# Performance work log

Measured on AMD Instinct MI355X. Metric: run time of the kernel, lower is better.

## Reference

```python
import jax, jax.numpy as jnp
import numpy as np
from jax import lax

D_MODEL = 512
N_HEADS = 8
D_HEAD = D_MODEL // N_HEADS
MAX_LANDMARKS = 100


def setup_inputs() -> dict:
    key = jax.random.key(0)
    ks = jax.random.split(key, 12)
    B, L, D = 16, 8192, D_MODEL
    s = 1.0 / np.sqrt(D)
    return {
        "mamba_output": jax.random.normal(ks[0], (B, L, D), jnp.float32),
        "hawkes_skip": jax.random.normal(ks[1], (B, L, D), jnp.float32),
        "hawkes_weights": jax.random.uniform(ks[2], (B, L), jnp.float32),
        "Wq": jax.random.uniform(ks[3], (D, D), jnp.float32, -s, s),
        "bq": jax.random.uniform(ks[4], (D,), jnp.float32, -s, s),
        "Wk": jax.random.uniform(ks[5], (D, D), jnp.float32, -s, s),
        "bk": jax.random.uniform(ks[6], (D,), jnp.float32, -s, s),
        "Wv": jax.random.uniform(ks[7], (D, D), jnp.float32, -s, s),
        "bv": jax.random.uniform(ks[8], (D,), jnp.float32, -s, s),
        "Wo": jax.random.uniform(ks[9], (D, D), jnp.float32, -s, s),
        "bo": jax.random.uniform(ks[10], (D,), jnp.float32, -s, s),
    }


def reference(mamba_output, hawkes_skip, hawkes_weights,
              Wq, bq, Wk, bk, Wv, bv, Wo, bo):
    B, L, D = hawkes_skip.shape
    H, dh = N_HEADS, D_HEAD
    k = min(MAX_LANDMARKS, L)
    scale = dh ** (-0.5)

    # top-k landmark selection over sequence, then chronological sort
    _, idx = lax.top_k(hawkes_weights, k)          # (B, k)
    idx = jnp.sort(idx, axis=1)
    landmark_kv = jnp.take_along_axis(hawkes_skip, idx[:, :, None], axis=1)  # (B, k, D)

    # single query = last timestep of mamba output
    query = mamba_output[:, -1, :]                 # (B, D)
    Q = (query @ Wq.T + bq).reshape(B, H, dh)      # (B, H, dh)
    K = (landmark_kv @ Wk.T + bk).reshape(B, k, H, dh)
    V = (landmark_kv @ Wv.T + bv).reshape(B, k, H, dh)

    scores = jnp.einsum("bhd,bkhd->bhk", Q, K) * scale   # (B, H, k)
    probs = jax.nn.softmax(scores, axis=-1)
    attn = jnp.einsum("bhk,bkhd->bhd", probs, V).reshape(B, D)
    return attn @ Wo.T + bo                        # (B, D)
```

## Files before the change

kernel.cpp:

```cpp
#include <hip/hip_runtime.h>
#include <hip/hip_bf16.h>
#include <stdint.h>

#define B_SZ 16
#define L_SEQ 8192
#define D_MOD 512
#define N_H 8
#define D_H 64
#define KSEL 100

__global__ __launch_bounds__(512) void fused_attn_kernel(
    const float* __restrict__ mamba, const float* __restrict__ skip,
    const float* __restrict__ w,
    const float* __restrict__ Wq, const float* __restrict__ bq,
    const float* __restrict__ Wk, const float* __restrict__ bk,
    const float* __restrict__ Wv, const float* __restrict__ bv,
    const float* __restrict__ Wo, const float* __restrict__ bo,
    float* __restrict__ out) {
    const int b = blockIdx.x >> 3;
    const int h = blockIdx.x & 7;
    const int t = threadIdx.x;
    const int lane = t & 63;
    const int wave = t >> 6;

    __shared__ uint32_t uval[L_SEQ];
    __shared__ float s_part[8 * D_MOD];
    __shared__ float s_query[D_MOD];
    __shared__ float s_a[D_MOD];
    __shared__ float s_y[D_MOD];
    __shared__ float s_Qh[D_H];
    __shared__ float s_ah[D_H];
    __shared__ int s_idx[128];
    __shared__ int s_eq[128];
    __shared__ int hist[256];
    __shared__ int s_wtot[4];
    __shared__ float s_m[8], s_l[8];
    __shared__ uint32_t s_thresh;
    __shared__ int s_rem, s_cnt, s_ecnt;
    __shared__ float s_qdotbk;

    const float* qrow = mamba + ((size_t)b * L_SEQ + (L_SEQ - 1)) * D_MOD;
    if (t < D_MOD) s_query[t] = qrow[t];
    const float* wb = w + (size_t)b * L_SEQ;
    for (int i = t; i < L_SEQ; i += 512) uval[i] = __float_as_uint(wb[i]);
    __syncthreads();

    const float* Wqh = Wq + (size_t)(h * D_H) * D_MOD;
    {
        const float4* q4 = (const float4*)s_query;
        float4 q0 = q4[lane * 2], q1 = q4[lane * 2 + 1];
        for (int d = wave; d < D_H; d += 8) {
            const float4* row4 = (const float4*)(Wqh + (size_t)d * D_MOD);
            float4 w0 = row4[lane * 2], w1 = row4[lane * 2 + 1];
            float sum = w0.x * q0.x + w0.y * q0.y + w0.z * q0.z + w0.w * q0.w +
                        w1.x * q1.x + w1.y * q1.y + w1.z * q1.z + w1.w * q1.w;
            #pragma unroll
            for (int off = 32; off > 0; off >>= 1) sum += __shfl_down(sum, off);
            if (lane == 0) s_Qh[d] = sum + bq[h * D_H + d];
        }
    }
    __syncthreads();

    if (wave == 0) {
        float v = s_Qh[lane] * bk[h * D_H + lane];
        #pragma unroll
        for (int off = 32; off > 0; off >>= 1) v += __shfl_down(v, off);
        if (lane == 0) s_qdotbk = v;
    }
    {
        const float* Wkh = Wk + (size_t)(h * D_H) * D_MOD;
        float4 a0 = {0, 0, 0, 0}, a1 = {0, 0, 0, 0};
        #pragma unroll
        for (int dd = 0; dd < 8; ++dd) {
            const int d = wave * 8 + dd;
            float qd = s_Qh[d];
            const float4* row4 = (const float4*)(Wkh + (size_t)d * D_MOD);
            float4 w0 = row4[lane * 2], w1 = row4[lane * 2 + 1];
            a0.x += qd * w0.x; a0.y += qd * w0.y; a0.z += qd * w0.z; a0.w += qd * w0.w;
            a1.x += qd * w1.x; a1.y += qd * w1.y; a1.z += qd * w1.z; a1.w += qd * w1.w;
        }
        float4* p4 = (float4*)&s_part[wave * D_MOD + lane * 8];
        p4[0] = a0; p4[1] = a1;
    }
    __syncthreads();
    {
        float v = 0.f;
        #pragma unroll
        for (int ww = 0; ww < 8; ++ww) v += s_part[ww * D_MOD + t];
        s_a[t] = v;
    }

    uint32_t prefix = 0, pmask = 0;
    int remaining = KSEL;
    for (int pass = 0; pass < 4; ++pass) {
        const int shift = 24 - 8 * pass;
        if (t < 256) hist[t] = 0;
        __syncthreads();
        for (int i = t; i < L_SEQ; i += 512) {
            uint32_t u = uval[i];
            if ((u & pmask) == prefix) atomicAdd(&hist[(u >> shift) & 0xFF], 1);
        }
        __syncthreads();
        int v = 0;
        if (t < 256) {
            v = hist[t];
            #pragma unroll
            for (int off = 1; off < 64; off <<= 1) {
                int u = __shfl_down(v, off);
                if (lane + off < 64) v += u;
            }
            if (lane == 0) s_wtot[wave] = v;
        }
        __syncthreads();
        if (t < 256) {
            int hi = 0;
            for (int w2 = wave + 1; w2 < 4; ++w2) hi += s_wtot[w2];
            int suff = v + hi;
            int suff_next = suff - hist[t];
            if (suff >= remaining && suff_next < remaining) {
                s_thresh = prefix | ((uint32_t)t << shift);
                s_rem = remaining - suff_next;
            }
        }
        __syncthreads();
        prefix = s_thresh;
        remaining = s_rem;
        pmask |= (uint32_t)0xFF << shift;
        __syncthreads();
    }

    if (t == 0) { s_cnt = 0; s_ecnt = 0; }
    __syncthreads();
    for (int i = t; i < L_SEQ; i += 512) {
        uint32_t u = uval[i];
        if (u > prefix) {
            int p = atomicAdd(&s_cnt, 1);
            s_idx[p] = i;
        } else if (u == prefix) {
            int p = atomicAdd(&s_ecnt, 1);
            if (p < 128) s_eq[p] = i;
        }
    }
    __syncthreads();
    const int cntgt = s_cnt;
    if (wave == 0) {
        int n = s_ecnt < 128 ? s_ecnt : 128;
        int taken_val = -1;
        for (int r = 0; r < remaining; ++r) {
            int mymin = 0x7FFFFFFF;
            for (int i = lane; i < n; i += 64) {
                int e = s_eq[i];
                if (e > taken_val && e < mymin) mymin = e;
            }
            #pragma unroll
            for (int off = 32; off > 0; off >>= 1) {
                int o = __shfl_xor(mymin, off);
                mymin = o < mymin ? o : mymin;
            }
            if (lane == 0) s_idx[cntgt + r] = mymin;
            taken_val = mymin;
        }
    }
    __syncthreads();

    const float scale = 0.125f;
    {
        const float4* a4 = (const float4*)s_a;
        float4 av0 = a4[lane * 2], av1 = a4[lane * 2 + 1];
        float qdotbk = s_qdotbk;
        float m = -INFINITY, l = 0.f;
        float4 acc0 = {0, 0, 0, 0}, acc1 = {0, 0, 0, 0};
        int j = wave;
        float4 x0 = {0, 0, 0, 0}, x1 = {0, 0, 0, 0};
        if (j < KSEL) {
            const float4* x4 =
                (const float4*)(skip + ((size_t)b * L_SEQ + s_idx[j]) * D_MOD);
            x0 = x4[lane * 2]; x1 = x4[lane * 2 + 1];
        }
        while (j < KSEL) {
            const int jn = j + 8;
            float4 n0 = {0, 0, 0, 0}, n1 = {0, 0, 0, 0};
            if (jn < KSEL) {
                const float4* x4 =
                    (const float4*)(skip + ((size_t)b * L_SEQ + s_idx[jn]) * D_MOD);
                n0 = x4[lane * 2]; n1 = x4[lane * 2 + 1];
            }
            float sum = x0.x * av0.x + x0.y * av0.y + x0.z * av0.z + x0.w * av0.w +
                        x1.x * av1.x + x1.y * av1.y + x1.z * av1.z + x1.w * av1.w;
            #pragma unroll
            for (int off = 32; off > 0; off >>= 1) sum += __shfl_xor(sum, off);
            float s = (sum + qdotbk) * scale;
            float mnew = fmaxf(m, s);
            float c = expf(m - mnew);
            float e = expf(s - mnew);
            l = l * c + e;
            acc0.x = acc0.x * c + e * x0.x; acc0.y = acc0.y * c + e * x0.y;
            acc0.z = acc0.z * c + e * x0.z; acc0.w = acc0.w * c + e * x0.w;
            acc1.x = acc1.x * c + e * x1.x; acc1.y = acc1.y * c + e * x1.y;
            acc1.z = acc1.z * c + e * x1.z; acc1.w = acc1.w * c + e * x1.w;
            m = mnew;
            x0 = n0; x1 = n1;
            j = jn;
        }
        float4* p4 = (float4*)&s_part[wave * D_MOD + lane * 8];
        p4[0] = acc0; p4[1] = acc1;
        if (lane == 0) { s_m[wave] = m; s_l[wave] = l; }
    }
    __syncthreads();

    {
        float mstar = -INFINITY;
        #pragma unroll
        for (int ww = 0; ww < 8; ++ww) mstar = fmaxf(mstar, s_m[ww]);
        float num = 0.f, den = 0.f;
        #pragma unroll
        for (int ww = 0; ww < 8; ++ww) {
            float sc = expf(s_m[ww] - mstar);
            num += sc * s_part[ww * D_MOD + t];
            den += sc * s_l[ww];
        }
        s_y[t] = num / den;
    }
    __syncthreads();

    const float* Wvh = Wv + (size_t)(h * D_H) * D_MOD;
    {
        const float4* y4 = (const float4*)s_y;
        float4 y0 = y4[lane * 2], y1 = y4[lane * 2 + 1];
        for (int d = wave; d < D_H; d += 8) {
            const float4* row4 = (const float4*)(Wvh + (size_t)d * D_MOD);
            float4 w0 = row4[lane * 2], w1 = row4[lane * 2 + 1];
            float sum = w0.x * y0.x + w0.y * y0.y + w0.z * y0.z + w0.w * y0.w +
                        w1.x * y1.x + w1.y * y1.y + w1.z * y1.z + w1.w * y1.w;
            #pragma unroll
            for (int off = 32; off > 0; off >>= 1) sum += __shfl_down(sum, off);
            if (lane == 0) s_ah[d] = sum + bv[h * D_H + d];
        }
    }
    __syncthreads();

    {
        const float4* wrow = (const float4*)(Wo + (size_t)t * D_MOD + h * D_H);
        const float4* ah4 = (const float4*)s_ah;
        float acc = 0.f;
        #pragma unroll
        for (int i = 0; i < 16; ++i) {
            float4 wv = wrow[i];
            float4 av = ah4[i];
            acc += wv.x * av.x + wv.y * av.y + wv.z * av.z + wv.w * av.w;
        }
        if (h == 0) acc += bo[t];
        atomicAdd(&out[(size_t)b * D_MOD + t], acc);
    }
}

extern "C" void kernel_launch(void* const* d_in, const int* in_sizes, int n_in,
                              void* d_out, int out_size, void* d_ws, size_t ws_size,
                              hipStream_t stream) {
    const float* mamba = (const float*)d_in[0];
    const float* skip  = (const float*)d_in[1];
    const float* hw    = (const float*)d_in[2];
    const float* Wq    = (const float*)d_in[3];
    const float* bq    = (const float*)d_in[4];
    const float* Wk    = (const float*)d_in[5];
    const float* bk    = (const float*)d_in[6];
    const float* Wv    = (const float*)d_in[7];
    const float* bv    = (const float*)d_in[8];
    const float* Wo    = (const float*)d_in[9];
    const float* bo    = (const float*)d_in[10];
    float* out = (float*)d_out;

    hipMemsetAsync(out, 0, (size_t)out_size * sizeof(float), stream);
    fused_attn_kernel<<<B_SZ * N_H, 512, 0, stream>>>(mamba, skip, hw, Wq, bq,
                                                      Wk, bk, Wv, bv, Wo, bo, out);
}
```

Baseline: 455.6 us.

## Prefetch weights into registers, privatize radix histograms, use exp2

Loads Wq/Wk rows into registers up front so they overlap with the hawkes-weight copy, and loads Wv/Wo rows during the attention loop so they are ready for the output projections. The radix-select histogram is split into 16 padded per-half-wave copies to reduce LDS atomic contention, and one barrier per pass is dropped. Softmax now uses exp2f with a log2e-folded scale. Holding these weights in registers raises register pressure at 512 threads and could spill or lower occupancy.

```diff
diff --git a/kernel.cpp b/kernel.cpp
--- a/kernel.cpp
+++ b/kernel.cpp
@@ -1,5 +1,4 @@
 #include <hip/hip_runtime.h>
-#include <hip/hip_bf16.h>
 #include <stdint.h>
 
 #define B_SZ 16
@@ -8,6 +7,8 @@
 #define N_H 8
 #define D_H 64
 #define KSEL 100
+#define HSUB 16
+#define HSTRIDE 258
 
 __global__ __launch_bounds__(512) void fused_attn_kernel(
     const float* __restrict__ mamba, const float* __restrict__ skip,
@@ -22,9 +23,11 @@
     const int t = threadIdx.x;
     const int lane = t & 63;
     const int wave = t >> 6;
+    const int sub = t >> 5;
 
     __shared__ uint32_t uval[L_SEQ];
     __shared__ float s_part[8 * D_MOD];
+    __shared__ int hist16[HSUB][HSTRIDE];
     __shared__ float s_query[D_MOD];
     __shared__ float s_a[D_MOD];
     __shared__ float s_y[D_MOD];
@@ -32,31 +35,49 @@
     __shared__ float s_ah[D_H];
     __shared__ int s_idx[128];
     __shared__ int s_eq[128];
-    __shared__ int hist[256];
     __shared__ int s_wtot[4];
     __shared__ float s_m[8], s_l[8];
     __shared__ uint32_t s_thresh;
     __shared__ int s_rem, s_cnt, s_ecnt;
     __shared__ float s_qdotbk;
 
+    if (t == 0) { s_cnt = 0; s_ecnt = 0; }
+
     const float* qrow = mamba + ((size_t)b * L_SEQ + (L_SEQ - 1)) * D_MOD;
-    if (t < D_MOD) s_query[t] = qrow[t];
-    const float* wb = w + (size_t)b * L_SEQ;
-    for (int i = t; i < L_SEQ; i += 512) uval[i] = __float_as_uint(wb[i]);
-    __syncthreads();
+    s_query[t] = qrow[t];
 
     const float* Wqh = Wq + (size_t)(h * D_H) * D_MOD;
+    const float* Wkh = Wk + (size_t)(h * D_H) * D_MOD;
+    float4 qw[8][2], kw[8][2];
+    #pragma unroll
+    for (int r = 0; r < 8; ++r) {
+        const float4* row4 = (const float4*)(Wqh + (size_t)(wave + r * 8) * D_MOD);
+        qw[r][0] = row4[lane * 2]; qw[r][1] = row4[lane * 2 + 1];
+    }
+    #pragma unroll
+    for (int dd = 0; dd < 8; ++dd) {
+        const float4* row4 = (const float4*)(Wkh + (size_t)(wave * 8 + dd) * D_MOD);
+        kw[dd][0] = row4[lane * 2]; kw[dd][1] = row4[lane * 2 + 1];
+    }
+    {
+        const uint4* wb4 = (const uint4*)(w + (size_t)b * L_SEQ);
+        uint4* uv4 = (uint4*)uval;
+        #pragma unroll
+        for (int i = 0; i < 4; ++i) uv4[t + i * 512] = wb4[t + i * 512];
+    }
+    __syncthreads();
+
     {
         const float4* q4 = (const float4*)s_query;
         float4 q0 = q4[lane * 2], q1 = q4[lane * 2 + 1];
-        for (int d = wave; d < D_H; d += 8) {
-            const float4* row4 = (const float4*)(Wqh + (size_t)d * D_MOD);
-            float4 w0 = row4[lane * 2], w1 = row4[lane * 2 + 1];
-            float sum = w0.x * q0.x + w0.y * q0.y + w0.z * q0.z + w0.w * q0.w +
-                        w1.x * q1.x + w1.y * q1.y + w1.z * q1.z + w1.w * q1.w;
+        #pragma unroll
+        for (int r = 0; r < 8; ++r) {
+            float sum = qw[r][0].x * q0.x + qw[r][0].y * q0.y + qw[r][0].z * q0.z +
+                        qw[r][0].w * q0.w + qw[r][1].x * q1.x + qw[r][1].y * q1.y +
+                        qw[r][1].z * q1.z + qw[r][1].w * q1.w;
             #pragma unroll
             for (int off = 32; off > 0; off >>= 1) sum += __shfl_down(sum, off);
-            if (lane == 0) s_Qh[d] = sum + bq[h * D_H + d];
+            if (lane == 0) s_Qh[wave + r * 8] = sum + bq[h * D_H + wave + r * 8];
         }
     }
     __syncthreads();
@@ -68,16 +89,14 @@
         if (lane == 0) s_qdotbk = v;
     }
     {
-        const float* Wkh = Wk + (size_t)(h * D_H) * D_MOD;
         float4 a0 = {0, 0, 0, 0}, a1 = {0, 0, 0, 0};
         #pragma unroll
         for (int dd = 0; dd < 8; ++dd) {
-            const int d = wave * 8 + dd;
-            float qd = s_Qh[d];
-            const float4* row4 = (const float4*)(Wkh + (size_t)d * D_MOD);
-            float4 w0 = row4[lane * 2], w1 = row4[lane * 2 + 1];
-            a0.x += qd * w0.x; a0.y += qd * w0.y; a0.z += qd * w0.z; a0.w += qd * w0.w;
-            a1.x += qd * w1.x; a1.y += qd * w1.y; a1.z += qd * w1.z; a1.w += qd * w1.w;
+            float qd = s_Qh[wave * 8 + dd];
+            a0.x += qd * kw[dd][0].x; a0.y += qd * kw[dd][0].y;
+            a0.z += qd * kw[dd][0].z; a0.w += qd * kw[dd][0].w;
+            a1.x += qd * kw[dd][1].x; a1.y += qd * kw[dd][1].y;
+            a1.z += qd * kw[dd][1].z; a1.w += qd * kw[dd][1].w;
         }
         float4* p4 = (float4*)&s_part[wave * D_MOD + lane * 8];
         p4[0] = a0; p4[1] = a1;
@@ -94,16 +113,18 @@
     int remaining = KSEL;
     for (int pass = 0; pass < 4; ++pass) {
         const int shift = 24 - 8 * pass;
-        if (t < 256) hist[t] = 0;
+        for (int i = t; i < HSUB * HSTRIDE; i += 512) ((int*)hist16)[i] = 0;
         __syncthreads();
         for (int i = t; i < L_SEQ; i += 512) {
             uint32_t u = uval[i];
-            if ((u & pmask) == prefix) atomicAdd(&hist[(u >> shift) & 0xFF], 1);
+            if ((u & pmask) == prefix) atomicAdd(&hist16[sub][(u >> shift) & 0xFF], 1);
         }
         __syncthreads();
-        int v = 0;
+        int binCount = 0, v = 0;
         if (t < 256) {
-            v = hist[t];
+            #pragma unroll
+            for (int s = 0; s < HSUB; ++s) binCount += hist16[s][t];
+            v = binCount;
             #pragma unroll
             for (int off = 1; off < 64; off <<= 1) {
                 int u = __shfl_down(v, off);
@@ -116,7 +137,7 @@
             int hi = 0;
             for (int w2 = wave + 1; w2 < 4; ++w2) hi += s_wtot[w2];
             int suff = v + hi;
-            int suff_next = suff - hist[t];
+            int suff_next = suff - binCount;
             if (suff >= remaining && suff_next < remaining) {
                 s_thresh = prefix | ((uint32_t)t << shift);
                 s_rem = remaining - suff_next;
@@ -126,11 +147,8 @@
         prefix = s_thresh;
         remaining = s_rem;
         pmask |= (uint32_t)0xFF << shift;
-        __syncthreads();
-    }
-
-    if (t == 0) { s_cnt = 0; s_ecnt = 0; }
-    __syncthreads();
+    }
+
     for (int i = t; i < L_SEQ; i += 512) {
         uint32_t u = uval[i];
         if (u > prefix) {
@@ -163,7 +181,10 @@
     }
     __syncthreads();
 
-    const float scale = 0.125f;
+    const float scale_l2e = 0.125f * 1.44269504088896340736f;
+    const float* Wvh = Wv + (size_t)(h * D_H) * D_MOD;
+    float4 vw[8][2];
+    float4 ow[16];
     {
         const float4* a4 = (const float4*)s_a;
         float4 av0 = a4[lane * 2], av1 = a4[lane * 2 + 1];
@@ -177,6 +198,16 @@
                 (const float4*)(skip + ((size_t)b * L_SEQ + s_idx[j]) * D_MOD);
             x0 = x4[lane * 2]; x1 = x4[lane * 2 + 1];
         }
+        #pragma unroll
+        for (int r = 0; r < 8; ++r) {
+            const float4* row4 = (const float4*)(Wvh + (size_t)(wave + r * 8) * D_MOD);
+            vw[r][0] = row4[lane * 2]; vw[r][1] = row4[lane * 2 + 1];
+        }
+        {
+            const float4* wrow = (const float4*)(Wo + (size_t)t * D_MOD + h * D_H);
+            #pragma unroll
+            for (int i = 0; i < 16; ++i) ow[i] = wrow[i];
+        }
         while (j < KSEL) {
             const int jn = j + 8;
             float4 n0 = {0, 0, 0, 0}, n1 = {0, 0, 0, 0};
@@ -189,10 +220,10 @@
                         x1.x * av1.x + x1.y * av1.y + x1.z * av1.z + x1.w * av1.w;
             #pragma unroll
             for (int off = 32; off > 0; off >>= 1) sum += __shfl_xor(sum, off);
-            float s = (sum + qdotbk) * scale;
+            float s = (sum + qdotbk) * scale_l2e;
             float mnew = fmaxf(m, s);
-            float c = expf(m - mnew);
-            float e = expf(s - mnew);
+            float c = exp2f(m - mnew);
+            float e = exp2f(s - mnew);
             l = l * c + e;
             acc0.x = acc0.x * c + e * x0.x; acc0.y = acc0.y * c + e * x0.y;
             acc0.z = acc0.z * c + e * x0.z; acc0.w = acc0.w * c + e * x0.w;
@@ -215,7 +246,7 @@
         float num = 0.f, den = 0.f;
         #pragma unroll
         for (int ww = 0; ww < 8; ++ww) {
-            float sc = expf(s_m[ww] - mstar);
+            float sc = exp2f(s_m[ww] - mstar);
             num += sc * s_part[ww * D_MOD + t];
             den += sc * s_l[ww];
         }
@@ -223,29 +254,27 @@
     }
     __syncthreads();
 
-    const float* Wvh = Wv + (size_t)(h * D_H) * D_MOD;
     {
         const float4* y4 = (const float4*)s_y;
         float4 y0 = y4[lane * 2], y1 = y4[lane * 2 + 1];
-        for (int d = wave; d < D_H; d += 8) {
-            const float4* row4 = (const float4*)(Wvh + (size_t)d * D_MOD);
-            float4 w0 = row4[lane * 2], w1 = row4[lane * 2 + 1];
-            float sum = w0.x * y0.x + w0.y * y0.y + w0.z * y0.z + w0.w * y0.w +
-                        w1.x * y1.x + w1.y * y1.y + w1.z * y1.z + w1.w * y1.w;
+        #pragma unroll
+        for (int r = 0; r < 8; ++r) {
+            float sum = vw[r][0].x * y0.x + vw[r][0].y * y0.y + vw[r][0].z * y0.z +
+                        vw[r][0].w * y0.w + vw[r][1].x * y1.x + vw[r][1].y * y1.y +
+                        vw[r][1].z * y1.z + vw[r][1].w * y1.w;
             #pragma unroll
             for (int off = 32; off > 0; off >>= 1) sum += __shfl_down(sum, off);
-            if (lane == 0) s_ah[d] = sum + bv[h * D_H + d];
-        }
-    }
-    __syncthreads();
-
-    {
-        const float4* wrow = (const float4*)(Wo + (size_t)t * D_MOD + h * D_H);
+            if (lane == 0) s_ah[wave + r * 8] = sum + bv[h * D_H + wave + r * 8];
+        }
+    }
+    __syncthreads();
+
+    {
         const float4* ah4 = (const float4*)s_ah;
         float acc = 0.f;
         #pragma unroll
         for (int i = 0; i < 16; ++i) {
-            float4 wv = wrow[i];
+            float4 wv = ow[i];
             float4 av = ah4[i];
             acc += wv.x * av.x + wv.y * av.y + wv.z * av.z + wv.w * av.w;
         }
```

Measured after the change: 449.8 us. Within noise of the previous version (-1.3%).
